# Kernel tuning notes

Measured on AMD Instinct MI355X. Metric: run time of the kernel, lower is better.

## Reference

```python
import jax, jax.numpy as jnp
import numpy as np

KH, KW = 3, 3
STRIDE = (1, 1)
PAD = (1, 1)
DIL = (1, 1)


def setup_inputs() -> dict:
    key = jax.random.key(0)
    k1, k2, k3, k4 = jax.random.split(key, 4)
    B, Cin, H, W = 8, 256, 64, 64
    Cout = 256
    x = jax.random.normal(k1, (B, Cin, H, W), jnp.float32)
    offset = jax.random.normal(k2, (B, 2 * KH * KW, H, W), jnp.float32)
    fan_in = Cin * KH * KW
    bound = 1.0 / np.sqrt(fan_in).astype(np.float32)
    weight = jax.random.uniform(k3, (Cout, Cin, KH, KW), jnp.float32, -bound, bound)
    bias = jax.random.uniform(k4, (Cout,), jnp.float32, -bound, bound)
    return {"x": x, "offset": offset, "weight": weight, "bias": bias}


def _deform_conv2d(x, offset, weight, bias):
    B, Cin, H, W = x.shape
    Cout = weight.shape[0]
    Ho, Wo = offset.shape[2], offset.shape[3]
    # offset layout: [B, 2*KH*KW, Ho, Wo] -> (dy, dx) per kernel tap
    off = offset.reshape(B, KH, KW, 2, Ho, Wo)
    dy = off[:, :, :, 0]  # [B,KH,KW,Ho,Wo]
    dx = off[:, :, :, 1]
    grid_y = jnp.arange(Ho, dtype=x.dtype) * STRIDE[0] - PAD[0]  # [Ho]
    grid_x = jnp.arange(Wo, dtype=x.dtype) * STRIDE[1] - PAD[1]  # [Wo]
    ker_y = jnp.arange(KH, dtype=x.dtype) * DIL[0]  # [KH]
    ker_x = jnp.arange(KW, dtype=x.dtype) * DIL[1]  # [KW]
    # sampling positions [B,KH,KW,Ho,Wo]
    py = dy + grid_y[None, None, None, :, None] + ker_y[None, :, None, None, None]
    px = dx + grid_x[None, None, None, None, :] + ker_x[None, None, :, None, None]

    y0f = jnp.floor(py)
    x0f = jnp.floor(px)
    wy = py - y0f  # fractional weights
    wx = px - x0f
    y0 = y0f.astype(jnp.int32)
    x0 = x0f.astype(jnp.int32)

    x_flat = x.reshape(B, Cin, H * W)

    def corner(yi, xi, w):
        # bilinear corner with zero padding outside the image
        valid = (yi >= 0) & (yi < H) & (xi >= 0) & (xi < W)
        idx = jnp.clip(yi, 0, H - 1) * W + jnp.clip(xi, 0, W - 1)  # [B,KH,KW,Ho,Wo]
        vals = jax.vmap(lambda xf, ii: xf[:, ii])(x_flat, idx)  # [B,Cin,KH,KW,Ho,Wo]
        return vals * (w * valid)[:, None]

    acc = corner(y0, x0, (1 - wy) * (1 - wx))
    acc = acc + corner(y0, x0 + 1, (1 - wy) * wx)
    acc = acc + corner(y0 + 1, x0, wy * (1 - wx))
    acc = acc + corner(y0 + 1, x0 + 1, wy * wx)

    # convolution accumulation over (Cin, KH, KW)
    out = jnp.einsum('bckluv,ockl->bouv', acc, weight)
    return out + bias[None, :, None, None]


def reference(x, offset, weight, bias):
    return _deform_conv2d(x, offset, weight, bias)
```

## Files before the change

### kernel.cpp

```cpp
#include <hip/hip_runtime.h>
#include <hip/hip_bf16.h>
#include <stdint.h>

typedef __attribute__((ext_vector_type(8))) short s16x8;
typedef __attribute__((ext_vector_type(4))) float f32x4;

#define XT_OFF   0u
#define WT_OFF   16777216u
#define PW_OFF   17956864u
#define PI_OFF   22675456u
#define WS_NEED  25034752u

static __device__ __forceinline__ uint16_t f2bf(float f) {
    __hip_bfloat16 h = __float2bfloat16(f);
    uint16_t u;
    __builtin_memcpy(&u, &h, 2);
    return u;
}
static __device__ __forceinline__ float bflo(uint32_t w) { return __uint_as_float(w << 16); }
static __device__ __forceinline__ float bfhi(uint32_t w) { return __uint_as_float(w & 0xffff0000u); }

__global__ __launch_bounds__(256) void k_transpose_x(const float* __restrict__ x,
                                                     uint16_t* __restrict__ xt) {
    __shared__ float tile[64][65];
    const int blk = blockIdx.x;
    const int b   = blk >> 8;
    const int yxt = (blk >> 2) & 63;
    const int ct  = blk & 3;
    const int yx0 = yxt << 6, c0 = ct << 6;
    const int tx  = threadIdx.x;
    const int ty  = tx >> 6, lx = tx & 63;
    #pragma unroll
    for (int i = 0; i < 16; ++i) {
        const int c = (i << 2) + ty;
        tile[c][lx] = x[(size_t)((b * 256 + c0 + c) << 12) + yx0 + lx];
    }
    __syncthreads();
    const int cpr = lx & 31;
    #pragma unroll
    for (int i = 0; i < 8; ++i) {
        const int r = (ty << 1) + (lx >> 5) + (i << 3);
        const uint32_t lo = f2bf(tile[2 * cpr][r]);
        const uint32_t hi = f2bf(tile[2 * cpr + 1][r]);
        *(uint32_t*)&xt[(size_t)(b * 4096 + yx0 + r) * 256 + c0 + 2 * cpr] = lo | (hi << 16);
    }
}

__global__ __launch_bounds__(256) void k_prep_w(const float* __restrict__ wgt,
                                                uint16_t* __restrict__ wt) {
    const int o = blockIdx.x;
    const int c = threadIdx.x;
    #pragma unroll
    for (int t = 0; t < 9; ++t) {
        const float v = wgt[(size_t)o * 2304 + c * 9 + t];
        const int kb = t * 8 + (c >> 5);
        const int kk = c & 31;
        const uint32_t byte = (uint32_t)kb * 16384u + (uint32_t)o * 64u
            + (uint32_t)(((((kk >> 3) ^ ((o >> 1) & 3)) << 4)) | ((kk & 7) << 1));
        wt[byte >> 1] = f2bf(v);
    }
}

__global__ __launch_bounds__(256) void k_prep_params(const float* __restrict__ off,
                                                     float4* __restrict__ pw,
                                                     uint2* __restrict__ pi) {
    const int blk = blockIdx.x;
    const int b = blk / 144;
    const int r = blk - b * 144;
    const int t = r >> 4;
    const int p = ((r & 15) << 8) + threadIdx.x;
    const int u = p >> 6, v = p & 63;
    const int kh = t / 3, kw = t - 3 * kh;
    const float dy = off[(size_t)((b * 18 + 2 * t) << 12) + p];
    const float dx = off[(size_t)((b * 18 + 2 * t + 1) << 12) + p];
    const float py = dy + (float)(u - 1 + kh);
    const float px = dx + (float)(v - 1 + kw);
    const float y0f = floorf(py), x0f = floorf(px);
    const float wy = py - y0f, wx = px - x0f;
    const int y0 = (int)y0f, x0 = (int)x0f;
    const int y1 = y0 + 1, x1 = x0 + 1;
    const bool vy0 = (y0 >= 0) && (y0 < 64);
    const bool vy1 = (y1 >= 0) && (y1 < 64);
    const bool vx0 = (x0 >= 0) && (x0 < 64);
    const bool vx1 = (x1 >= 0) && (x1 < 64);
    const int cy0 = min(max(y0, 0), 63), cy1 = min(max(y1, 0), 63);
    const int cx0 = min(max(x0, 0), 63), cx1 = min(max(x1, 0), 63);
    float4 w4;
    w4.x = (1.f - wy) * (1.f - wx) * ((vy0 && vx0) ? 1.f : 0.f);
    w4.y = (1.f - wy) * wx         * ((vy0 && vx1) ? 1.f : 0.f);
    w4.z = wy * (1.f - wx)         * ((vy1 && vx0) ? 1.f : 0.f);
    w4.w = wy * wx                 * ((vy1 && vx1) ? 1.f : 0.f);
    uint2 id;
    id.x = (uint32_t)(cy0 * 64 + cx0) | ((uint32_t)(cy0 * 64 + cx1) << 16);
    id.y = (uint32_t)(cy1 * 64 + cx0) | ((uint32_t)(cy1 * 64 + cx1) << 16);
    const size_t o_ = (size_t)(b * 9 + t) * 4096 + p;
    pw[o_] = w4;
    pi[o_] = id;
}

__global__ __launch_bounds__(512, 4) void k_main(const uint16_t* __restrict__ xt,
                                                 const uint16_t* __restrict__ wt,
                                                 const float4* __restrict__ pw,
                                                 const uint2* __restrict__ pi,
                                                 const float* __restrict__ bias,
                                                 float* __restrict__ out) {
    __shared__ uint16_t w_lds[2][8192];
    __shared__ uint16_t im2col[64 * 256];

    const int orig = blockIdx.x;
    const int bid  = (orig & 7) * 64 + (orig >> 3);
    const int b    = bid >> 6;
    const int pix0 = (bid & 63) << 6;

    const int tx   = threadIdx.x;
    const int lane = tx & 63;
    const int wv   = tx >> 6;
    const int wc   = wv & 3;
    const int wp   = wv >> 2;
    const int l15  = lane & 15;
    const int kp   = lane >> 4;

    const int ar    = wc * 64 + l15;
    const int a_off = ar * 64 + ((kp ^ ((ar >> 1) & 3)) << 4);

    const uint16_t* xb = xt + (size_t)b * 4096 * 256;

    f32x4 acc[4][2];
    #pragma unroll
    for (int m = 0; m < 4; ++m)
        #pragma unroll
        for (int j = 0; j < 2; ++j) acc[m][j] = (f32x4){0.f, 0.f, 0.f, 0.f};

    for (int t = 0; t < 9; ++t) {
        __syncthreads();
        {
            const char* gw = (const char*)wt + (size_t)(t * 8) * 16384u;
            char* lw = (char*)&w_lds[0][0];
            #pragma unroll
            for (int it = 0; it < 2; ++it) {
                const int seg = wv * 2 + it;
                __builtin_amdgcn_global_load_lds(
                    (const __attribute__((address_space(1))) void*)(gw + seg * 1024 + lane * 16),
                    (__attribute__((address_space(3))) void*)(lw + seg * 1024), 16, 0, 0);
            }
        }
        #pragma unroll
        for (int i = 0; i < 8; ++i) {
            const int lp = wv * 8 + i;
            const int uidx = __builtin_amdgcn_readfirstlane((b * 9 + t) * 4096 + pix0 + lp);
            const uint2  id = pi[uidx];
            const float4 w4 = pw[uidx];
            const uint16_t* p00 = xb + (id.x & 0xffffu) * 256u;
            const uint16_t* p01 = xb + (id.x >> 16)     * 256u;
            const uint16_t* p10 = xb + (id.y & 0xffffu) * 256u;
            const uint16_t* p11 = xb + (id.y >> 16)     * 256u;
            const uint2 A  = *(const uint2*)(p00 + lane * 4);
            const uint2 Bv = *(const uint2*)(p01 + lane * 4);
            const uint2 Cv = *(const uint2*)(p10 + lane * 4);
            const uint2 Dv = *(const uint2*)(p11 + lane * 4);
            uint2 r;
            {
                const float lo = w4.x * bflo(A.x) + w4.y * bflo(Bv.x)
                               + w4.z * bflo(Cv.x) + w4.w * bflo(Dv.x);
                const float hi = w4.x * bfhi(A.x) + w4.y * bfhi(Bv.x)
                               + w4.z * bfhi(Cv.x) + w4.w * bfhi(Dv.x);
                r.x = (uint32_t)f2bf(lo) | ((uint32_t)f2bf(hi) << 16);
            }
            {
                const float lo = w4.x * bflo(A.y) + w4.y * bflo(Bv.y)
                               + w4.z * bflo(Cv.y) + w4.w * bflo(Dv.y);
                const float hi = w4.x * bfhi(A.y) + w4.y * bfhi(Bv.y)
                               + w4.z * bfhi(Cv.y) + w4.w * bfhi(Dv.y);
                r.y = (uint32_t)f2bf(lo) | ((uint32_t)f2bf(hi) << 16);
            }
            const int slot = (lane >> 1) ^ (lp & 7);
            *(uint2*)((char*)im2col + lp * 512 + slot * 16 + (lane & 1) * 8) = r;
        }
        __syncthreads();

        #pragma unroll
        for (int s = 0; s < 8; ++s) {
            const int kb = t * 8 + s;
            if (kb + 1 < 72) {
                const char* gw = (const char*)wt + (size_t)(kb + 1) * 16384u;
                char* lw = (char*)&w_lds[(s + 1) & 1][0];
                #pragma unroll
                for (int it = 0; it < 2; ++it) {
                    const int seg = wv * 2 + it;
                    __builtin_amdgcn_global_load_lds(
                        (const __attribute__((address_space(1))) void*)(gw + seg * 1024 + lane * 16),
                        (__attribute__((address_space(3))) void*)(lw + seg * 1024), 16, 0, 0);
                }
            }
            const char* wb = (const char*)&w_lds[s & 1][0];
            s16x8 afr[4], bfr[2];
            #pragma unroll
            for (int m = 0; m < 4; ++m) afr[m] = *(const s16x8*)(wb + a_off + m * 1024);
            #pragma unroll
            for (int j = 0; j < 2; ++j) {
                const int pix  = wp * 32 + j * 16 + l15;
                const int boff = pix * 512 + (((s * 4 + kp) ^ (l15 & 7)) << 4);
                bfr[j] = *(const s16x8*)((const char*)im2col + boff);
            }
            #pragma unroll
            for (int m = 0; m < 4; ++m)
                #pragma unroll
                for (int j = 0; j < 2; ++j)
                    acc[m][j] = __builtin_amdgcn_mfma_f32_16x16x32_bf16(afr[m], bfr[j], acc[m][j], 0, 0, 0);
            __syncthreads();
        }
    }

    #pragma unroll
    for (int m = 0; m < 4; ++m) {
        #pragma unroll
        for (int q = 0; q < 4; ++q) {
            const int o = wc * 64 + m * 16 + kp * 4 + q;
            const float bv = bias[o];
            float* orow = out + (((size_t)(b * 256 + o)) << 12) + pix0 + wp * 32;
            #pragma unroll
            for (int j = 0; j < 2; ++j)
                orow[j * 16 + l15] = acc[m][j][q] + bv;
        }
    }
}

#define KTOT 2304
#define KCF  32
#define WROW 260
#define AROW 72

__global__ __launch_bounds__(256) void deform_conv_fallback(
    const float* __restrict__ x, const float* __restrict__ off,
    const float* __restrict__ wgt, const float* __restrict__ bias,
    float* __restrict__ out) {
    __shared__ float  w_lds[KCF][WROW];
    __shared__ float  a_lds[KCF][AROW];
    __shared__ int4   pidx[9][64];
    __shared__ float4 pwgt[9][64];
    const int tx = threadIdx.x;
    const int blk = blockIdx.x;
    const int b = blk >> 6, u = blk & 63;
    for (int item = tx; item < 9 * 64; item += 256) {
        const int t = item >> 6, p = item & 63;
        const int k = t / 3, l = t - 3 * k;
        const float dy = off[((b * 18 + 2 * t) << 12) + u * 64 + p];
        const float dx = off[((b * 18 + 2 * t + 1) << 12) + u * 64 + p];
        const float py = dy + (float)(u - 1 + k);
        const float px = dx + (float)(p - 1 + l);
        const float y0f = floorf(py), x0f = floorf(px);
        const float wy = py - y0f, wx = px - x0f;
        const int y0 = (int)y0f, x0 = (int)x0f, y1 = y0 + 1, x1 = x0 + 1;
        const bool vy0 = (y0 >= 0) && (y0 < 64), vy1 = (y1 >= 0) && (y1 < 64);
        const bool vx0 = (x0 >= 0) && (x0 < 64), vx1 = (x1 >= 0) && (x1 < 64);
        const int cy0 = min(max(y0, 0), 63), cy1 = min(max(y1, 0), 63);
        const int cx0 = min(max(x0, 0), 63), cx1 = min(max(x1, 0), 63);
        int4 id; id.x = cy0 * 64 + cx0; id.y = cy0 * 64 + cx1;
        id.z = cy1 * 64 + cx0; id.w = cy1 * 64 + cx1;
        float4 w4;
        w4.x = (1.f - wy) * (1.f - wx) * ((vy0 && vx0) ? 1.f : 0.f);
        w4.y = (1.f - wy) * wx * ((vy0 && vx1) ? 1.f : 0.f);
        w4.z = wy * (1.f - wx) * ((vy1 && vx0) ? 1.f : 0.f);
        w4.w = wy * wx * ((vy1 && vx1) ? 1.f : 0.f);
        pidx[t][p] = id; pwgt[t][p] = w4;
    }
    const int og = tx & 31, pgr = tx >> 5;
    float acc[8][8];
    #pragma unroll
    for (int j = 0; j < 8; ++j)
        #pragma unroll
        for (int q = 0; q < 8; ++q) acc[j][q] = 0.f;
    __syncthreads();
    for (int kb = 0; kb < 72; ++kb) {
        const int k0 = kb * KCF;
        #pragma unroll
        for (int it = 0; it < 8; ++it) {
            const int item = it * 256 + tx;
            const int o = item >> 3, jj = item & 7;
            const float4 v = *(const float4*)&wgt[o * KTOT + k0 + jj * 4];
            w_lds[jj * 4 + 0][o] = v.x; w_lds[jj * 4 + 1][o] = v.y;
            w_lds[jj * 4 + 2][o] = v.z; w_lds[jj * 4 + 3][o] = v.w;
        }
        #pragma unroll
        for (int it = 0; it < 8; ++it) {
            const int item = it * 256 + tx;
            const int kk = item >> 6, p = item & 63;
            const int kg = k0 + kk;
            const int c = kg / 9, t = kg - 9 * c;
            const float* plane = x + ((b * 256 + c) << 12);
            const int4 id = pidx[t][p];
            const float4 w4 = pwgt[t][p];
            float v = w4.x * plane[id.x] + w4.y * plane[id.y]
                    + w4.z * plane[id.z] + w4.w * plane[id.w];
            a_lds[kk][p] = v;
        }
        __syncthreads();
        #pragma unroll 2
        for (int kk = 0; kk < KCF; ++kk) {
            const float4 w0 = *(const float4*)&w_lds[kk][og * 8];
            const float4 w1 = *(const float4*)&w_lds[kk][og * 8 + 4];
            const float4 a0 = *(const float4*)&a_lds[kk][pgr * 8];
            const float4 a1 = *(const float4*)&a_lds[kk][pgr * 8 + 4];
            const float wv[8] = {w0.x, w0.y, w0.z, w0.w, w1.x, w1.y, w1.z, w1.w};
            const float av[8] = {a0.x, a0.y, a0.z, a0.w, a1.x, a1.y, a1.z, a1.w};
            #pragma unroll
            for (int j = 0; j < 8; ++j)
                #pragma unroll
                for (int q = 0; q < 8; ++q) acc[j][q] += wv[j] * av[q];
        }
        __syncthreads();
    }
    const int vb = pgr * 8;
    #pragma unroll
    for (int j = 0; j < 8; ++j) {
        const int o = og * 8 + j;
        const float bv = bias[o];
        float* op = out + ((b * 256 + o) << 12) + u * 64 + vb;
        float4 r0, r1;
        r0.x = acc[j][0] + bv; r0.y = acc[j][1] + bv; r0.z = acc[j][2] + bv; r0.w = acc[j][3] + bv;
        r1.x = acc[j][4] + bv; r1.y = acc[j][5] + bv; r1.z = acc[j][6] + bv; r1.w = acc[j][7] + bv;
        *(float4*)op = r0; *(float4*)(op + 4) = r1;
    }
}

extern "C" void kernel_launch(void* const* d_in, const int* in_sizes, int n_in,
                              void* d_out, int out_size, void* d_ws, size_t ws_size,
                              hipStream_t stream) {
    const float* x    = (const float*)d_in[0];
    const float* off  = (const float*)d_in[1];
    const float* wgt  = (const float*)d_in[2];
    const float* bias = (const float*)d_in[3];
    float* out = (float*)d_out;

    if (ws_size < WS_NEED) {
        deform_conv_fallback<<<dim3(512), dim3(256), 0, stream>>>(x, off, wgt, bias, out);
        return;
    }
    uint16_t* xt  = (uint16_t*)((char*)d_ws + XT_OFF);
    uint16_t* wtp = (uint16_t*)((char*)d_ws + WT_OFF);
    float4*   pwp = (float4*)((char*)d_ws + PW_OFF);
    uint2*    pip = (uint2*)((char*)d_ws + PI_OFF);

    k_transpose_x <<<dim3(2048), dim3(256), 0, stream>>>(x, xt);
    k_prep_w      <<<dim3(256),  dim3(256), 0, stream>>>(wgt, wtp);
    k_prep_params <<<dim3(1152), dim3(256), 0, stream>>>(off, pwp, pip);
    k_main        <<<dim3(512),  dim3(512), 0, stream>>>(xt, wtp, pwp, pip, bias, out);
}
```

Before: 100.3 us.

## Triple-buffer weight tiles with prefetch distance two and explicit waitcnt barriers

Weight slabs now go through three LDS buffers, prefetched two k-blocks ahead, instead of double-buffered one ahead. The redundant reload of each tap's first weight block at the start of every tap loop is dropped. The trailing __syncthreads is replaced by a leading s_waitcnt vmcnt(2) plus s_barrier, so the newest DMA can stay in flight. MFMA issue is wrapped in s_setprio to favour the matrix work. The cost is extra LDS per block, which may affect occupancy at 4 blocks per CU, and correctness now depends on hand-written waitcnt counts.

```diff
diff --git a/kernel.cpp b/kernel.cpp
--- a/kernel.cpp
+++ b/kernel.cpp
@@ -98,13 +98,25 @@
     pi[o_] = id;
 }
 
+#define W_DMA(KB, BUF) do {                                                       \
+    const char* gw_ = (const char*)wt + (size_t)(KB) * 16384u;                    \
+    char* lw_ = (char*)&w_lds[BUF][0];                                            \
+    _Pragma("unroll")                                                             \
+    for (int it_ = 0; it_ < 2; ++it_) {                                           \
+        const int seg_ = wv * 2 + it_;                                            \
+        __builtin_amdgcn_global_load_lds(                                         \
+            (const __attribute__((address_space(1))) void*)(gw_ + seg_ * 1024 + lane * 16), \
+            (__attribute__((address_space(3))) void*)(lw_ + seg_ * 1024), 16, 0, 0); \
+    }                                                                             \
+} while (0)
+
 __global__ __launch_bounds__(512, 4) void k_main(const uint16_t* __restrict__ xt,
                                                  const uint16_t* __restrict__ wt,
                                                  const float4* __restrict__ pw,
                                                  const uint2* __restrict__ pi,
                                                  const float* __restrict__ bias,
                                                  float* __restrict__ out) {
-    __shared__ uint16_t w_lds[2][8192];
+    __shared__ uint16_t w_lds[3][8192];
     __shared__ uint16_t im2col[64 * 256];
 
     const int orig = blockIdx.x;
@@ -131,19 +143,11 @@
         #pragma unroll
         for (int j = 0; j < 2; ++j) acc[m][j] = (f32x4){0.f, 0.f, 0.f, 0.f};
 
+    W_DMA(0, 0);
+    W_DMA(1, 1);
+
     for (int t = 0; t < 9; ++t) {
         __syncthreads();
-        {
-            const char* gw = (const char*)wt + (size_t)(t * 8) * 16384u;
-            char* lw = (char*)&w_lds[0][0];
-            #pragma unroll
-            for (int it = 0; it < 2; ++it) {
-                const int seg = wv * 2 + it;
-                __builtin_amdgcn_global_load_lds(
-                    (const __attribute__((address_space(1))) void*)(gw + seg * 1024 + lane * 16),
-                    (__attribute__((address_space(3))) void*)(lw + seg * 1024), 16, 0, 0);
-            }
-        }
         #pragma unroll
         for (int i = 0; i < 8; ++i) {
             const int lp = wv * 8 + i;
@@ -181,18 +185,16 @@
         #pragma unroll
         for (int s = 0; s < 8; ++s) {
             const int kb = t * 8 + s;
-            if (kb + 1 < 72) {
-                const char* gw = (const char*)wt + (size_t)(kb + 1) * 16384u;
-                char* lw = (char*)&w_lds[(s + 1) & 1][0];
-                #pragma unroll
-                for (int it = 0; it < 2; ++it) {
-                    const int seg = wv * 2 + it;
-                    __builtin_amdgcn_global_load_lds(
-                        (const __attribute__((address_space(1))) void*)(gw + seg * 1024 + lane * 16),
-                        (__attribute__((address_space(3))) void*)(lw + seg * 1024), 16, 0, 0);
-                }
+            if (t == 8 && s == 7) asm volatile("s_waitcnt vmcnt(0) lgkmcnt(0)" ::: "memory");
+            else                  asm volatile("s_waitcnt vmcnt(2) lgkmcnt(0)" ::: "memory");
+            __builtin_amdgcn_s_barrier();
+            __builtin_amdgcn_sched_barrier(0);
+            if (kb + 2 < 72) {
+                const int ib = (kb + 2) % 3;
+                W_DMA(kb + 2, ib);
             }
-            const char* wb = (const char*)&w_lds[s & 1][0];
+            const int cb = kb % 3;
+            const char* wb = (const char*)&w_lds[cb][0];
             s16x8 afr[4], bfr[2];
             #pragma unroll
             for (int m = 0; m < 4; ++m) afr[m] = *(const s16x8*)(wb + a_off + m * 1024);
@@ -202,12 +204,13 @@
                 const int boff = pix * 512 + (((s * 4 + kp) ^ (l15 & 7)) << 4);
                 bfr[j] = *(const s16x8*)((const char*)im2col + boff);
             }
+            __builtin_amdgcn_s_setprio(1);
             #pragma unroll
             for (int m = 0; m < 4; ++m)
                 #pragma unroll
                 for (int j = 0; j < 2; ++j)
                     acc[m][j] = __builtin_amdgcn_mfma_f32_16x16x32_bf16(afr[m], bfr[j], acc[m][j], 0, 0, 0);
-            __syncthreads();
+            __builtin_amdgcn_s_setprio(0);
         }
     }
 
```

After: 98.86 us. Within noise of the previous version (-1.4%).
